# Performance work log

Measured on AMD Instinct MI355X. Metric: run time of the kernel, lower is better.

The kernel has to match this reference:

```python
import jax, jax.numpy as jnp
import numpy as np

L, ND, ED = 1024, 64, 32  # seq len, node_embedding_dim, edge_embedding_dim
LN_EPS = 1e-5  # haiku LayerNorm default


def setup_inputs() -> dict:
    key = jax.random.key(0)
    ks = jax.random.split(key, 8)
    node_features = jax.random.normal(ks[0], (L, ND), dtype=jnp.float32)
    pair_features = jax.random.normal(ks[1], (L, L, ED), dtype=jnp.float32)
    # hk.Linear(ED) over concat([node_i, node_j, pair]) -> fan_in = 2*ND + ED
    fan_pair = 2 * ND + ED
    W_pair = jax.random.normal(ks[2], (fan_pair, ED), dtype=jnp.float32) / np.sqrt(fan_pair)
    b_pair = jnp.zeros((ED,), dtype=jnp.float32)
    # hk.Linear(ND) over concat([node, pair_to_node]) -> fan_in = ND + ED
    fan_node = ND + ED
    W_node = jax.random.normal(ks[3], (fan_node, ND), dtype=jnp.float32) / np.sqrt(fan_node)
    b_node = jnp.zeros((ND,), dtype=jnp.float32)
    ln_scale = jnp.ones((ND,), dtype=jnp.float32)
    ln_offset = jnp.zeros((ND,), dtype=jnp.float32)
    return {
        "node_features": node_features,
        "pair_features": pair_features,
        "W_pair": W_pair,
        "b_pair": b_pair,
        "W_node": W_node,
        "b_node": b_node,
        "ln_scale": ln_scale,
        "ln_offset": ln_offset,
    }


def reference(node_features, pair_features, W_pair, b_pair, W_node, b_node, ln_scale, ln_offset):
    # Pair update: Linear(concat([bcast node_i, bcast node_j, pair])).
    # Split the weight into node_i / node_j / pair blocks so we never
    # materialize the (L, L, 2*ND+ED) concat tensor -- same math.
    Wi = W_pair[:ND]          # (ND, ED)
    Wj = W_pair[ND:2 * ND]    # (ND, ED)
    Wp = W_pair[2 * ND:]      # (ED, ED)
    ni = node_features @ Wi   # (L, ED)
    nj = node_features @ Wj   # (L, ED)
    pair_update = (ni[:, None, :] + nj[None, :, :]
                   + jnp.einsum('ije,ef->ijf', pair_features, Wp) + b_pair)
    pair_out = pair_features + pair_update                      # (L, L, ED)

    # Node update: mean over axis=1, concat, linear, residual, LayerNorm.
    pair_to_node = jnp.mean(pair_out, axis=1)                   # (L, ED)
    node_in = jnp.concatenate([node_features, pair_to_node], axis=-1)  # (L, ND+ED)
    node = node_features + node_in @ W_node + b_node            # (L, ND)

    mean = jnp.mean(node, axis=-1, keepdims=True)
    var = jnp.var(node, axis=-1, keepdims=True)
    node = (node - mean) * jax.lax.rsqrt(var + LN_EPS) * ln_scale + ln_offset
    return node, pair_out
```

## Files before the change

### kernel.cpp

```cpp
#include <hip/hip_runtime.h>
#include <stdint.h>

#define LSEQ 1024
#define EDIM 32
#define NDIM 64

typedef __attribute__((ext_vector_type(8))) short short8;
typedef __attribute__((ext_vector_type(4))) float f32x4;

static __device__ __forceinline__ unsigned short f2bf(float f) {
    unsigned int u = __float_as_uint(f);
    u += 0x7FFFu + ((u >> 16) & 1u);
    return (unsigned short)(u >> 16);
}

__global__ __launch_bounds__(256) void evo_pre(
    const float* __restrict__ node,
    const float* __restrict__ Wpair,
    const float* __restrict__ bpair,
    float* __restrict__ niB,
    float* __restrict__ njB,
    unsigned short* __restrict__ wpT)
{
    int g = blockIdx.x * 256 + threadIdx.x;
    if (g < LSEQ * EDIM) {
        int i = g >> 5, f = g & 31;
        float acci = bpair[f];
        float accj = 0.0f;
        const float* nrow = node + i * NDIM;
        #pragma unroll
        for (int k = 0; k < NDIM; ++k) {
            float nv = nrow[k];
            acci += nv * Wpair[k * 32 + f];
            accj += nv * Wpair[(64 + k) * 32 + f];
        }
        niB[g] = acci;
        njB[g] = accj;
    } else {
        int idx = g - LSEQ * EDIM;
        if (idx < EDIM * EDIM) {
            int f = idx >> 5, e = idx & 31;
            float v = Wpair[(128 + e) * 32 + f];
            if (e == f) v += 1.0f;
            wpT[f * 32 + e] = f2bf(v);
        }
    }
}

__global__ __launch_bounds__(256) void evo_main(
    const float* __restrict__ pair,
    const float* __restrict__ node,
    const float* __restrict__ niB,
    const float* __restrict__ njB,
    const unsigned short* __restrict__ wpT,
    const float* __restrict__ Wnode,
    const float* __restrict__ bnode,
    const float* __restrict__ lnsc,
    const float* __restrict__ lnof,
    float* __restrict__ out_node,
    float* __restrict__ out_pair)
{
    __shared__ float red[4][32];
    __shared__ float p2n[32];
    __shared__ float node_f[64];

    const int i    = blockIdx.x;
    const int tid  = threadIdx.x;
    const int wave = tid >> 6;
    const int lane = tid & 63;
    const int c    = lane & 15;
    const int a    = lane >> 4;

    if (tid < 64) node_f[tid] = node[i * 64 + tid];

    const short8 af0 = *(const short8*)(wpT + c * 32 + a * 8);
    const short8 af1 = *(const short8*)(wpT + (c + 16) * 32 + a * 8);
    const f32x4 ni0 = *(const f32x4*)(niB + i * 32 + 4 * a);
    const f32x4 ni1 = *(const f32x4*)(niB + i * 32 + 4 * a + 16);

    f32x4 sum0 = {0.f, 0.f, 0.f, 0.f};
    f32x4 sum1 = {0.f, 0.f, 0.f, 0.f};
    const size_t rowbase = ((size_t)i) << 10;

    for (int t = 0; t < 16; ++t) {
        const int jr = (wave << 8) + (t << 4) + c;
        const size_t pbase = (rowbase + jr) << 5;
        const f32x4 pa = *(const f32x4*)(pair + pbase + a * 8);
        const f32x4 pb = *(const f32x4*)(pair + pbase + a * 8 + 4);
        short8 bfrag;
        bfrag[0] = (short)f2bf(pa.x); bfrag[1] = (short)f2bf(pa.y);
        bfrag[2] = (short)f2bf(pa.z); bfrag[3] = (short)f2bf(pa.w);
        bfrag[4] = (short)f2bf(pb.x); bfrag[5] = (short)f2bf(pb.y);
        bfrag[6] = (short)f2bf(pb.z); bfrag[7] = (short)f2bf(pb.w);
        const f32x4 z = {0.f, 0.f, 0.f, 0.f};
        f32x4 acc0 = __builtin_amdgcn_mfma_f32_16x16x32_bf16(af0, bfrag, z, 0, 0, 0);
        f32x4 acc1 = __builtin_amdgcn_mfma_f32_16x16x32_bf16(af1, bfrag, z, 0, 0, 0);
        const f32x4 nj0 = *(const f32x4*)(njB + jr * 32 + 4 * a);
        const f32x4 nj1 = *(const f32x4*)(njB + jr * 32 + 4 * a + 16);
        const f32x4 o0 = acc0 + ni0 + nj0;
        const f32x4 o1 = acc1 + ni1 + nj1;
        sum0 += o0;
        sum1 += o1;
        *(f32x4*)(out_pair + pbase + 4 * a)      = o0;
        *(f32x4*)(out_pair + pbase + 4 * a + 16) = o1;
    }

    for (int m = 1; m < 16; m <<= 1) {
        sum0.x += __shfl_xor(sum0.x, m); sum0.y += __shfl_xor(sum0.y, m);
        sum0.z += __shfl_xor(sum0.z, m); sum0.w += __shfl_xor(sum0.w, m);
        sum1.x += __shfl_xor(sum1.x, m); sum1.y += __shfl_xor(sum1.y, m);
        sum1.z += __shfl_xor(sum1.z, m); sum1.w += __shfl_xor(sum1.w, m);
    }
    if (c == 0) {
        red[wave][4 * a + 0]      = sum0.x;
        red[wave][4 * a + 1]      = sum0.y;
        red[wave][4 * a + 2]      = sum0.z;
        red[wave][4 * a + 3]      = sum0.w;
        red[wave][16 + 4 * a + 0] = sum1.x;
        red[wave][16 + 4 * a + 1] = sum1.y;
        red[wave][16 + 4 * a + 2] = sum1.z;
        red[wave][16 + 4 * a + 3] = sum1.w;
    }
    __syncthreads();
    if (tid < 32) {
        p2n[tid] = (red[0][tid] + red[1][tid] + red[2][tid] + red[3][tid]) * (1.0f / 1024.0f);
    }
    __syncthreads();

    if (tid < 64) {
        float acc = node_f[tid] + bnode[tid];
        #pragma unroll 8
        for (int k = 0; k < 64; ++k)
            acc += node_f[k] * Wnode[k * 64 + tid];
        #pragma unroll 8
        for (int k = 0; k < 32; ++k)
            acc += p2n[k] * Wnode[(64 + k) * 64 + tid];
        float s = acc, s2 = acc * acc;
        for (int m = 1; m < 64; m <<= 1) {
            s  += __shfl_xor(s, m);
            s2 += __shfl_xor(s2, m);
        }
        const float mean = s * (1.0f / 64.0f);
        const float var  = s2 * (1.0f / 64.0f) - mean * mean;
        const float y = (acc - mean) * rsqrtf(var + 1e-5f) * lnsc[tid] + lnof[tid];
        out_node[i * 64 + tid] = y;
    }
}

extern "C" void kernel_launch(void* const* d_in, const int* in_sizes, int n_in,
                              void* d_out, int out_size, void* d_ws, size_t ws_size,
                              hipStream_t stream) {
    const float* node  = (const float*)d_in[0];
    const float* pair  = (const float*)d_in[1];
    const float* Wpair = (const float*)d_in[2];
    const float* bpair = (const float*)d_in[3];
    const float* Wnode = (const float*)d_in[4];
    const float* bnode = (const float*)d_in[5];
    const float* lnsc  = (const float*)d_in[6];
    const float* lnof  = (const float*)d_in[7];

    float* niB = (float*)d_ws;
    float* njB = niB + LSEQ * EDIM;
    unsigned short* wpT = (unsigned short*)(njB + LSEQ * EDIM);

    float* out_node = (float*)d_out;
    float* out_pair = out_node + LSEQ * NDIM;

    evo_pre<<<132, 256, 0, stream>>>(node, Wpair, bpair, niB, njB, wpT);
    evo_main<<<LSEQ, 256, 0, stream>>>(pair, node, niB, njB, wpT,
                                       Wnode, bnode, lnsc, lnof,
                                       out_node, out_pair);
}
```

Baseline: 68.36 us.

## Split each pair row across two blocks, prefetch loads, move node update to separate kernel

```diff
diff --git a/kernel.cpp b/kernel.cpp
--- a/kernel.cpp
+++ b/kernel.cpp
@@ -47,31 +47,24 @@
     }
 }
 
-__global__ __launch_bounds__(256) void evo_main(
+__global__ __launch_bounds__(256, 8) void evo_main(
     const float* __restrict__ pair,
-    const float* __restrict__ node,
     const float* __restrict__ niB,
     const float* __restrict__ njB,
     const unsigned short* __restrict__ wpT,
-    const float* __restrict__ Wnode,
-    const float* __restrict__ bnode,
-    const float* __restrict__ lnsc,
-    const float* __restrict__ lnof,
-    float* __restrict__ out_node,
+    float* __restrict__ partial,
     float* __restrict__ out_pair)
 {
     __shared__ float red[4][32];
-    __shared__ float p2n[32];
-    __shared__ float node_f[64];
 
-    const int i    = blockIdx.x;
+    const int blk  = blockIdx.x;
+    const int i    = blk >> 1;
+    const int h    = blk & 1;
     const int tid  = threadIdx.x;
     const int wave = tid >> 6;
     const int lane = tid & 63;
     const int c    = lane & 15;
     const int a    = lane >> 4;
-
-    if (tid < 64) node_f[tid] = node[i * 64 + tid];
 
     const short8 af0 = *(const short8*)(wpT + c * 32 + a * 8);
     const short8 af1 = *(const short8*)(wpT + (c + 16) * 32 + a * 8);
@@ -80,13 +73,22 @@
 
     f32x4 sum0 = {0.f, 0.f, 0.f, 0.f};
     f32x4 sum1 = {0.f, 0.f, 0.f, 0.f};
-    const size_t rowbase = ((size_t)i) << 10;
 
-    for (int t = 0; t < 16; ++t) {
-        const int jr = (wave << 8) + (t << 4) + c;
-        const size_t pbase = (rowbase + jr) << 5;
-        const f32x4 pa = *(const f32x4*)(pair + pbase + a * 8);
-        const f32x4 pb = *(const f32x4*)(pair + pbase + a * 8 + 4);
+    const int jw = (h << 9) + (wave << 7);
+    const size_t base = ((((size_t)i) << 10) + (size_t)(jw + c)) << 5;
+    const float* pin  = pair + base + a * 8;
+    const float* njp  = njB + (size_t)(jw + c) * 32 + 4 * a;
+    float*       pout = out_pair + base + 4 * a;
+
+    f32x4 pa = *(const f32x4*)(pin);
+    f32x4 pb = *(const f32x4*)(pin + 4);
+
+    #pragma unroll
+    for (int t = 0; t < 8; ++t) {
+        const int tn = (t < 7) ? (t + 1) : 7;
+        const f32x4 na = *(const f32x4*)(pin + tn * 512);
+        const f32x4 nb = *(const f32x4*)(pin + tn * 512 + 4);
+
         short8 bfrag;
         bfrag[0] = (short)f2bf(pa.x); bfrag[1] = (short)f2bf(pa.y);
         bfrag[2] = (short)f2bf(pa.z); bfrag[3] = (short)f2bf(pa.w);
@@ -95,14 +97,16 @@
         const f32x4 z = {0.f, 0.f, 0.f, 0.f};
         f32x4 acc0 = __builtin_amdgcn_mfma_f32_16x16x32_bf16(af0, bfrag, z, 0, 0, 0);
         f32x4 acc1 = __builtin_amdgcn_mfma_f32_16x16x32_bf16(af1, bfrag, z, 0, 0, 0);
-        const f32x4 nj0 = *(const f32x4*)(njB + jr * 32 + 4 * a);
-        const f32x4 nj1 = *(const f32x4*)(njB + jr * 32 + 4 * a + 16);
+        const f32x4 nj0 = *(const f32x4*)(njp + t * 512);
+        const f32x4 nj1 = *(const f32x4*)(njp + t * 512 + 16);
         const f32x4 o0 = acc0 + ni0 + nj0;
         const f32x4 o1 = acc1 + ni1 + nj1;
         sum0 += o0;
         sum1 += o1;
-        *(f32x4*)(out_pair + pbase + 4 * a)      = o0;
-        *(f32x4*)(out_pair + pbase + 4 * a + 16) = o1;
+        *(f32x4*)(pout + t * 512)      = o0;
+        *(f32x4*)(pout + t * 512 + 16) = o1;
+        pa = na;
+        pb = nb;
     }
 
     for (int m = 1; m < 16; m <<= 1) {
@@ -123,28 +127,48 @@
     }
     __syncthreads();
     if (tid < 32) {
-        p2n[tid] = (red[0][tid] + red[1][tid] + red[2][tid] + red[3][tid]) * (1.0f / 1024.0f);
+        partial[blk * 32 + tid] = red[0][tid] + red[1][tid] + red[2][tid] + red[3][tid];
+    }
+}
+
+__global__ __launch_bounds__(64) void evo_finish(
+    const float* __restrict__ node,
+    const float* __restrict__ partial,
+    const float* __restrict__ Wnode,
+    const float* __restrict__ bnode,
+    const float* __restrict__ lnsc,
+    const float* __restrict__ lnof,
+    float* __restrict__ out_node)
+{
+    __shared__ float node_f[64];
+    __shared__ float p2n[32];
+    const int i   = blockIdx.x;
+    const int tid = threadIdx.x;
+
+    node_f[tid] = node[i * 64 + tid];
+    if (tid < 32) {
+        p2n[tid] = (partial[(2 * i) * 32 + tid] + partial[(2 * i + 1) * 32 + tid])
+                   * (1.0f / 1024.0f);
     }
     __syncthreads();
 
-    if (tid < 64) {
-        float acc = node_f[tid] + bnode[tid];
-        #pragma unroll 8
-        for (int k = 0; k < 64; ++k)
-            acc += node_f[k] * Wnode[k * 64 + tid];
-        #pragma unroll 8
-        for (int k = 0; k < 32; ++k)
-            acc += p2n[k] * Wnode[(64 + k) * 64 + tid];
-        float s = acc, s2 = acc * acc;
-        for (int m = 1; m < 64; m <<= 1) {
-            s  += __shfl_xor(s, m);
-            s2 += __shfl_xor(s2, m);
-        }
-        const float mean = s * (1.0f / 64.0f);
-        const float var  = s2 * (1.0f / 64.0f) - mean * mean;
-        const float y = (acc - mean) * rsqrtf(var + 1e-5f) * lnsc[tid] + lnof[tid];
-        out_node[i * 64 + tid] = y;
+    float acc = node_f[tid] + bnode[tid];
+    #pragma unroll 8
+    for (int k = 0; k < 64; ++k)
+        acc += node_f[k] * Wnode[k * 64 + tid];
+    #pragma unroll 8
+    for (int k = 0; k < 32; ++k)
+        acc += p2n[k] * Wnode[(64 + k) * 64 + tid];
+
+    float s = acc, s2 = acc * acc;
+    for (int m = 1; m < 64; m <<= 1) {
+        s  += __shfl_xor(s, m);
+        s2 += __shfl_xor(s2, m);
     }
+    const float mean = s * (1.0f / 64.0f);
+    const float var  = s2 * (1.0f / 64.0f) - mean * mean;
+    const float y = (acc - mean) * rsqrtf(var + 1e-5f) * lnsc[tid] + lnof[tid];
+    out_node[i * 64 + tid] = y;
 }
 
 extern "C" void kernel_launch(void* const* d_in, const int* in_sizes, int n_in,
@@ -162,12 +186,13 @@
     float* niB = (float*)d_ws;
     float* njB = niB + LSEQ * EDIM;
     unsigned short* wpT = (unsigned short*)(njB + LSEQ * EDIM);
+    float* partial = (float*)(wpT + EDIM * EDIM);
 
     float* out_node = (float*)d_out;
     float* out_pair = out_node + LSEQ * NDIM;
 
     evo_pre<<<132, 256, 0, stream>>>(node, Wpair, bpair, niB, njB, wpT);
-    evo_main<<<LSEQ, 256, 0, stream>>>(pair, node, niB, njB, wpT,
-                                       Wnode, bnode, lnsc, lnof,
-                                       out_node, out_pair);
+    evo_main<<<2 * LSEQ, 256, 0, stream>>>(pair, niB, njB, wpT, partial, out_pair);
+    evo_finish<<<LSEQ, 64, 0, stream>>>(node, partial, Wnode, bnode, lnsc, lnof,
+                                        out_node);
 }
```

Measured after the change: 96.93 us. +41.8%, slower.
